# Kernel tuning notes

Measured on AMD Instinct MI355X. Metric: run time of the kernel, lower is better.

Reference implementation:

```python
import jax, jax.numpy as jnp
import numpy as np

MAX_LEN_PROP = 0.75
SCORE_STDDEV = 3.0


def setup_inputs() -> dict:
    key = jax.random.key(0)
    k0, k1, k2, k3, k4, k5 = jax.random.split(key, 6)
    F, B, C = 4096, 32, 512
    x = jax.random.normal(k0, (F, B, C), dtype=jnp.float32)
    lengths = jax.random.randint(k1, (B,), 0, F, dtype=jnp.int32)
    rand_u = jax.random.uniform(k2, (F // 2, B, 1), dtype=jnp.float32)
    W = jax.random.normal(k3, (2, C), dtype=jnp.float32) * 0.02
    b = jax.random.normal(k4, (2,), dtype=jnp.float32) * 0.02
    is_sep = jax.random.normal(k5, (C,), dtype=jnp.float32) * 0.01
    return {"x": x, "lengths": lengths, "rand_u": rand_u, "W": W, "b": b, "is_sep": is_sep}


def reference(x, lengths, rand_u, W, b, is_sep):
    F, B, C = x.shape
    newF = int(1 + F * MAX_LEN_PROP)

    # per-pair loss prediction on even frames: (F/2, B, 2)
    pred = jnp.einsum('fbc,oc->fbo', x[0::2], W) + b

    # normalize scores to target stddev (std over frame axis), negate
    centered = pred - jnp.mean(pred, axis=-1, keepdims=True)
    std = jnp.sqrt(jnp.mean(centered ** 2, axis=0, keepdims=True) + 1e-20)
    scores = centered * (-SCORE_STDDEV / std)
    probs = jax.nn.softmax(scores, axis=-1)

    kept = probs[..., 0:1] > rand_u                       # (F/2, B, 1) bool
    sel = (~kept).astype(jnp.int32)                       # gather index: 0 if kept else 1
    seq_losses = jnp.take_along_axis(pred, sel, axis=2)[..., 0].sum(axis=0)  # (B,)

    lengths_mask = jnp.arange(F)[:, None, None] < lengths[None, :, None]     # (F, B, 1)
    ones = lengths_mask.astype(jnp.int32)
    ones = ones.at[0::2].multiply(kept.astype(jnp.int32))  # drop non-kept even frames

    indexes = jnp.cumsum(ones, axis=0)                     # inclusive cumsum (F, B, 1)
    new_lengths = jnp.minimum(indexes[-1, :, 0], newF)     # (B,)
    indexes = indexes - ones                               # exclusive cumsum = write index

    ones_f = ones.astype(x.dtype)
    pair_mean = ones_f.reshape(F // 2, 2, B, 1).mean(axis=1, keepdims=True)
    scales = jnp.broadcast_to(pair_mean, (F // 2, 2, B, 1)).reshape(F, B, 1)
    scales = jnp.where(indexes >= newF, jnp.zeros((), x.dtype), scales)

    idx = jnp.minimum(indexes, newF - 1)[..., 0]           # (F, B)
    bidx = jnp.arange(B)[None, :]

    # scatter-add compacted, scaled frames into shrunk buffer
    y = jnp.zeros((newF, B, C), x.dtype).at[idx, bidx].add(x * scales)

    kept_dup = jnp.broadcast_to(kept.reshape(F // 2, 1, B, 1), (F // 2, 2, B, 1)).reshape(F, B, 1)
    kept_dup = kept_dup.astype(x.dtype) * lengths_mask.astype(x.dtype)
    is_sep_acc = jnp.zeros((newF, B), x.dtype).at[idx, bidx].add(kept_dup[..., 0])

    y = y + is_sep_acc[..., None] * is_sep
    return y, new_lengths, seq_losses
```

## Files before the change

kernel.cpp:

```cpp
#include <hip/hip_runtime.h>
#include <math.h>

#define FF 4096
#define NPAIR 2048
#define BB 32
#define CC 512
#define NEWF 3073

typedef float f32x4 __attribute__((ext_vector_type(4)));

__global__ __launch_bounds__(256) void pred_kernel(
    const float* __restrict__ x, const float* __restrict__ W,
    const float* __restrict__ bias, double* __restrict__ pred) {
  int wave = threadIdx.x >> 6;
  int lane = threadIdx.x & 63;
  int row  = blockIdx.x * 4 + wave;
  int f2 = row >> 5;
  int b  = row & 31;
  const float* xr = x + ((size_t)(2 * f2) * BB + b) * CC;

  double s0 = 0.0, s1 = 0.0;
#pragma unroll
  for (int k = 0; k < 2; ++k) {
    int c = lane * 4 + k * 256;
    f32x4 xv = *(const f32x4*)(xr + c);
    f32x4 w0 = *(const f32x4*)(W + c);
    f32x4 w1 = *(const f32x4*)(W + CC + c);
    s0 += (double)xv.x * (double)w0.x + (double)xv.y * (double)w0.y +
          (double)xv.z * (double)w0.z + (double)xv.w * (double)w0.w;
    s1 += (double)xv.x * (double)w1.x + (double)xv.y * (double)w1.y +
          (double)xv.z * (double)w1.z + (double)xv.w * (double)w1.w;
  }
#pragma unroll
  for (int off = 32; off; off >>= 1) {
    s0 += __shfl_down(s0, off, 64);
    s1 += __shfl_down(s1, off, 64);
  }
  if (lane == 0) {
    size_t o = ((size_t)b * NPAIR + f2) * 2;
    pred[o + 0] = s0 + (double)bias[0];
    pred[o + 1] = s1 + (double)bias[1];
  }
}

__global__ __launch_bounds__(1024) void scan_kernel(
    const double* __restrict__ pred, const float* __restrict__ rand_u,
    const int* __restrict__ lengths, int* __restrict__ rec,
    int* __restrict__ tail, float* __restrict__ out_tail) {
  int b = blockIdx.x;
  int t = threadIdx.x;
  int lane = t & 63, wid = t >> 6;

  __shared__ double wdbl[16];
  __shared__ int    wint[16];
  __shared__ double s_invs;

  int len = lengths[b];
  const double* pb = pred + (size_t)b * NPAIR * 2;

  int pr0 = 2 * t, pr1 = 2 * t + 1;
  double2 a0 = ((const double2*)pb)[2 * t];
  double2 a1 = ((const double2*)pb)[2 * t + 1];
  float ru0 = rand_u[(size_t)pr0 * BB + b];
  float ru1 = rand_u[(size_t)pr1 * BB + b];
  double d0 = a0.x - a0.y;
  double d1 = a1.x - a1.y;

  double sumsq = 0.25 * (d0 * d0 + d1 * d1);
#pragma unroll
  for (int off = 32; off; off >>= 1) sumsq += __shfl_down(sumsq, off, 64);
  if (lane == 0) wdbl[wid] = sumsq;
  __syncthreads();
  if (t == 0) {
    double s = 0;
#pragma unroll
    for (int i = 0; i < 16; ++i) s += wdbl[i];
    s_invs = -3.0 / sqrt(s / (double)NPAIR + 1e-20);
  }
  __syncthreads();
  double si = s_invs;

  double prob0 = 1.0 / (1.0 + exp(-d0 * si));
  double prob1 = 1.0 / (1.0 + exp(-d1 * si));
  bool kept0 = prob0 > (double)ru0;
  bool kept1 = prob1 > (double)ru1;
  bool oe0 = (2 * pr0 < len) && kept0;
  bool oo0 = (2 * pr0 + 1) < len;
  bool oe1 = (2 * pr1 < len) && kept1;
  bool oo1 = (2 * pr1 + 1) < len;
  int cnt = (int)oe0 + (int)oo0 + (int)oe1 + (int)oo1;

  int sc = cnt;
#pragma unroll
  for (int off = 1; off < 64; off <<= 1) {
    int v = __shfl_up(sc, off, 64);
    if (lane >= off) sc += v;
  }
  if (lane == 63) wint[wid] = sc;
  __syncthreads();
  int wprefix = 0, total = 0;
#pragma unroll
  for (int i = 0; i < 16; ++i) {
    int wv = wint[i];
    if (i < wid) wprefix += wv;
    total += wv;
  }
  int base = wprefix + sc - cnt;

  int* rrow = rec + (size_t)b * NEWF;
  int zstart = total < NEWF ? total : NEWF;
  for (int s = zstart + t; s < NEWF; s += 1024) rrow[s] = 0;
  __syncthreads();

  int excl = base;
  int tailc = 0;
  double seq = (kept0 ? a0.x : a0.y) + (kept1 ? a1.x : a1.y);

#pragma unroll
  for (int i = 0; i < 2; ++i) {
    int pr = 2 * t + i;
    bool kept = i ? kept1 : kept0;
    bool oe = i ? oe1 : oe0;
    bool oo = i ? oo1 : oo0;
    int fe = 2 * pr, fo = fe + 1;
    int excl_e = excl; excl += (int)oe;
    int excl_o = excl; excl += (int)oo;

    if (oe) {
      if (excl_e < NEWF) {
        int half = oo ? 0 : 1;
        rrow[excl_e] = 1 | (half << 2) | (1 << 3) | (fe << 4);
      }
      if (excl_e >= NEWF - 1) tailc++;
    }
    if (oo) {
      if (excl_o < NEWF) {
        int two  = kept ? 0 : 1;
        int half = kept ? 0 : 1;
        rrow[excl_o] = 1 | (two << 1) | (half << 2) | ((kept ? 1 : 0) << 3) | (fo << 4);
      }
      if (kept && excl_o >= NEWF - 1) tailc++;
    }
    if (!oo && oe && excl_o < NEWF) {
      rrow[excl_o] = 1 | (1 << 2) | (fo << 4);
    }
  }

#pragma unroll
  for (int off = 32; off; off >>= 1) {
    seq   += __shfl_down(seq, off, 64);
    tailc += __shfl_down(tailc, off, 64);
  }
  __syncthreads();
  if (lane == 0) { wdbl[wid] = seq; wint[wid] = tailc; }
  __syncthreads();
  if (t == 0) {
    double ss = 0; int tc = 0;
#pragma unroll
    for (int i = 0; i < 16; ++i) { ss += wdbl[i]; tc += wint[i]; }
    tail[b] = tc;
    out_tail[b]      = (float)(total < NEWF ? total : NEWF);
    out_tail[BB + b] = (float)ss;
  }
}

__global__ __launch_bounds__(128) void gather_kernel(
    const float* __restrict__ x, const int* __restrict__ rec,
    const int* __restrict__ tail, const float* __restrict__ is_sep,
    float* __restrict__ y) {
  int s = blockIdx.x;
  int b = blockIdx.y;
  int r = rec[(size_t)b * NEWF + s];
  int c = threadIdx.x * 4;

  int cv = (s == NEWF - 1) ? tail[b] : ((r >> 3) & 1);

  f32x4 acc = (f32x4)(0.f);
  if (r & 1) {
    int f = r >> 4;
    float sc = (r & 4) ? 0.5f : 1.0f;
    f32x4 xv = *(const f32x4*)(x + ((size_t)f * BB + b) * CC + c);
    acc = sc * xv;
    if (r & 2) {
      f32x4 x2 = *(const f32x4*)(x + ((size_t)(f - 1) * BB + b) * CC + c);
      acc += 0.5f * x2;
    }
  }
  if (cv) {
    f32x4 is = *(const f32x4*)(is_sep + c);
    acc += (float)cv * is;
  }
  __builtin_nontemporal_store(acc, (f32x4*)(y + ((size_t)s * BB + b) * CC + c));
}

extern "C" void kernel_launch(void* const* d_in, const int* in_sizes, int n_in,
                              void* d_out, int out_size, void* d_ws, size_t ws_size,
                              hipStream_t stream) {
  (void)in_sizes; (void)n_in; (void)out_size; (void)ws_size;
  const float* x       = (const float*)d_in[0];
  const int*   lengths = (const int*)d_in[1];
  const float* rand_u  = (const float*)d_in[2];
  const float* W       = (const float*)d_in[3];
  const float* bias    = (const float*)d_in[4];
  const float* is_sep  = (const float*)d_in[5];

  float* y = (float*)d_out;
  float* out_tail = y + (size_t)NEWF * BB * CC;

  char* ws = (char*)d_ws;
  double* pred = (double*)ws;
  int* rec  = (int*)(ws + (size_t)BB * NPAIR * 2 * sizeof(double));
  int* tail = rec + (size_t)BB * NEWF;

  pred_kernel<<<(NPAIR * BB) / 4, 256, 0, stream>>>(x, W, bias, pred);
  scan_kernel<<<BB, 1024, 0, stream>>>(pred, rand_u, lengths, rec, tail, out_tail);
  gather_kernel<<<dim3(NEWF, BB), 128, 0, stream>>>(x, rec, tail, is_sep, y);
}
```

Measured before the change: 75.07 us.

## Fuse pred, scan and gather into one persistent cooperative kernel

Merges the three launches into one cooperative kernel that computes predictions grid-stride, syncs the grid, runs the per-batch scan on 32 blocks, syncs again, then gathers output rows in a persistent loop. It is meant to remove launch gaps and inter-kernel idle time. In exchange, most blocks idle during the scan, grid-wide barriers add cost, and the persistent gather loop may keep fewer memory requests in flight. The old three-kernel path remains as a fallback if the cooperative launch fails.

After: 223.4 us. 198% more time.

```diff
diff --git a/kernel.cpp b/kernel.cpp
--- a/kernel.cpp
+++ b/kernel.cpp
@@ -1,13 +1,206 @@
 #include <hip/hip_runtime.h>
+#include <hip/hip_cooperative_groups.h>
 #include <math.h>
+
+namespace cg = cooperative_groups;
 
 #define FF 4096
 #define NPAIR 2048
 #define BB 32
 #define CC 512
 #define NEWF 3073
+#define NROWS (NPAIR * BB)
+#define TPB 256
 
 typedef float f32x4 __attribute__((ext_vector_type(4)));
+
+__device__ inline double dot4d(f32x4 a, f32x4 w) {
+  return (double)a.x * (double)w.x + (double)a.y * (double)w.y +
+         (double)a.z * (double)w.z + (double)a.w * (double)w.w;
+}
+
+__global__ __launch_bounds__(TPB, 2) void fused_kernel(
+    const float* __restrict__ x, const int* __restrict__ lengths,
+    const float* __restrict__ rand_u, const float* __restrict__ W,
+    const float* __restrict__ bias, const float* __restrict__ is_sep,
+    double* __restrict__ pred, int* __restrict__ rec, int* __restrict__ tail,
+    float* __restrict__ y, float* __restrict__ out_tail) {
+  cg::grid_group grid = cg::this_grid();
+  int bid = blockIdx.x;
+  int tid = threadIdx.x;
+  int lane = tid & 63;
+  int wid = tid >> 6;
+
+  {
+    int c0 = lane * 4, c1 = lane * 4 + 256;
+    f32x4 w00 = *(const f32x4*)(W + c0);
+    f32x4 w01 = *(const f32x4*)(W + c1);
+    f32x4 w10 = *(const f32x4*)(W + CC + c0);
+    f32x4 w11 = *(const f32x4*)(W + CC + c1);
+    double bb0 = (double)bias[0], bb1 = (double)bias[1];
+    int nw = gridDim.x * 4;
+    int wgid = bid * 4 + wid;
+    for (int row = wgid; row < NROWS; row += nw) {
+      int f2 = row >> 5, b = row & 31;
+      const float* xr = x + ((size_t)(2 * f2) * BB + b) * CC;
+      f32x4 xv0 = *(const f32x4*)(xr + c0);
+      f32x4 xv1 = *(const f32x4*)(xr + c1);
+      double s0 = dot4d(xv0, w00) + dot4d(xv1, w01);
+      double s1 = dot4d(xv0, w10) + dot4d(xv1, w11);
+#pragma unroll
+      for (int off = 32; off; off >>= 1) {
+        s0 += __shfl_down(s0, off, 64);
+        s1 += __shfl_down(s1, off, 64);
+      }
+      if (lane == 0) {
+        double2 pv; pv.x = s0 + bb0; pv.y = s1 + bb1;
+        ((double2*)pred)[(size_t)b * NPAIR + f2] = pv;
+      }
+    }
+  }
+  grid.sync();
+
+  if (bid < BB) {
+    __shared__ double sh_d[4];
+    __shared__ int    sh_i[4];
+    __shared__ int    sh_s[4];
+    __shared__ double s_invs;
+    int b = bid;
+    int len = lengths[b];
+    const double* pb = pred + (size_t)b * NPAIR * 2;
+
+    double d[8];
+    double sumsq = 0.0;
+#pragma unroll
+    for (int i = 0; i < 8; ++i) {
+      double2 a = ((const double2*)pb)[tid * 8 + i];
+      d[i] = a.x - a.y;
+      sumsq += 0.25 * d[i] * d[i];
+    }
+#pragma unroll
+    for (int off = 32; off; off >>= 1) sumsq += __shfl_down(sumsq, off, 64);
+    if (lane == 0) sh_d[wid] = sumsq;
+    __syncthreads();
+    if (tid == 0)
+      s_invs = -3.0 / sqrt((sh_d[0] + sh_d[1] + sh_d[2] + sh_d[3]) /
+                               (double)NPAIR + 1e-20);
+    __syncthreads();
+    double si = s_invs;
+
+    int keptm = 0, oem = 0, oom = 0, cnt = 0;
+#pragma unroll
+    for (int i = 0; i < 8; ++i) {
+      int pr = tid * 8 + i;
+      double prob = 1.0 / (1.0 + exp(-d[i] * si));
+      bool kept = prob > (double)rand_u[(size_t)pr * BB + b];
+      bool oe = (2 * pr < len) && kept;
+      bool oo = (2 * pr + 1) < len;
+      if (kept) keptm |= 1 << i;
+      if (oe) oem |= 1 << i;
+      if (oo) oom |= 1 << i;
+      cnt += (int)oe + (int)oo;
+    }
+
+    int sc = cnt;
+#pragma unroll
+    for (int off = 1; off < 64; off <<= 1) {
+      int v = __shfl_up(sc, off, 64);
+      if (lane >= off) sc += v;
+    }
+    if (lane == 63) sh_s[wid] = sc;
+    __syncthreads();
+    int wpre = 0, total = 0;
+#pragma unroll
+    for (int i = 0; i < 4; ++i) {
+      if (i < wid) wpre += sh_s[i];
+      total += sh_s[i];
+    }
+    int base = wpre + sc - cnt;
+
+    int* rrow = rec + (size_t)b * NEWF;
+    int zstart = total < NEWF ? total : NEWF;
+    for (int s = zstart + tid; s < NEWF; s += TPB) rrow[s] = 0;
+    __syncthreads();
+
+    int excl = base, tailc = 0;
+    double seq = 0.0;
+#pragma unroll
+    for (int i = 0; i < 8; ++i) {
+      int pr = tid * 8 + i;
+      double2 a = ((const double2*)pb)[pr];
+      bool kept = (keptm >> i) & 1;
+      bool oe = (oem >> i) & 1;
+      bool oo = (oom >> i) & 1;
+      seq += kept ? a.x : a.y;
+      int fe = 2 * pr, fo = fe + 1;
+      int excl_e = excl; excl += (int)oe;
+      int excl_o = excl; excl += (int)oo;
+
+      if (oe) {
+        if (excl_e < NEWF) {
+          int half = oo ? 0 : 1;
+          rrow[excl_e] = 1 | (half << 2) | (1 << 3) | (fe << 4);
+        }
+        if (excl_e >= NEWF - 1) tailc++;
+      }
+      if (oo) {
+        if (excl_o < NEWF) {
+          int two  = kept ? 0 : 1;
+          int half = kept ? 0 : 1;
+          rrow[excl_o] = 1 | (two << 1) | (half << 2) | ((kept ? 1 : 0) << 3) | (fo << 4);
+        }
+        if (kept && excl_o >= NEWF - 1) tailc++;
+      }
+      if (!oo && oe && excl_o < NEWF) {
+        rrow[excl_o] = 1 | (1 << 2) | (fo << 4);
+      }
+    }
+
+#pragma unroll
+    for (int off = 32; off; off >>= 1) {
+      seq   += __shfl_down(seq, off, 64);
+      tailc += __shfl_down(tailc, off, 64);
+    }
+    __syncthreads();
+    if (lane == 0) { sh_d[wid] = seq; sh_i[wid] = tailc; }
+    __syncthreads();
+    if (tid == 0) {
+      tail[b] = sh_i[0] + sh_i[1] + sh_i[2] + sh_i[3];
+      out_tail[b]      = (float)(total < NEWF ? total : NEWF);
+      out_tail[BB + b] = (float)(sh_d[0] + sh_d[1] + sh_d[2] + sh_d[3]);
+    }
+  }
+  grid.sync();
+
+  {
+    int nh = gridDim.x * 2;
+    int hid = bid * 2 + (tid >> 7);
+    int c = (tid & 127) * 4;
+    f32x4 isv = *(const f32x4*)(is_sep + c);
+    int b = 0, s = hid;
+    while (b < BB) {
+      int r = rec[(size_t)b * NEWF + s];
+      int cv = (s == NEWF - 1) ? tail[b] : ((r >> 3) & 1);
+
+      f32x4 acc = (f32x4)(0.f);
+      if (r & 1) {
+        int f = r >> 4;
+        float scv = (r & 4) ? 0.5f : 1.0f;
+        f32x4 xv = *(const f32x4*)(x + ((size_t)f * BB + b) * CC + c);
+        acc = scv * xv;
+        if (r & 2) {
+          f32x4 x2 = *(const f32x4*)(x + ((size_t)(f - 1) * BB + b) * CC + c);
+          acc += 0.5f * x2;
+        }
+      }
+      if (cv) acc += (float)cv * isv;
+      __builtin_nontemporal_store(acc, (f32x4*)(y + ((size_t)s * BB + b) * CC + c));
+
+      s += nh;
+      if (s >= NEWF) { s -= NEWF; b++; }
+    }
+  }
+}
 
 __global__ __launch_bounds__(256) void pred_kernel(
     const float* __restrict__ x, const float* __restrict__ W,
@@ -26,10 +219,8 @@
     f32x4 xv = *(const f32x4*)(xr + c);
     f32x4 w0 = *(const f32x4*)(W + c);
     f32x4 w1 = *(const f32x4*)(W + CC + c);
-    s0 += (double)xv.x * (double)w0.x + (double)xv.y * (double)w0.y +
-          (double)xv.z * (double)w0.z + (double)xv.w * (double)w0.w;
-    s1 += (double)xv.x * (double)w1.x + (double)xv.y * (double)w1.y +
-          (double)xv.z * (double)w1.z + (double)xv.w * (double)w1.w;
+    s0 += dot4d(xv, w0);
+    s1 += dot4d(xv, w1);
   }
 #pragma unroll
   for (int off = 32; off; off >>= 1) {
@@ -178,9 +369,9 @@
   f32x4 acc = (f32x4)(0.f);
   if (r & 1) {
     int f = r >> 4;
-    float sc = (r & 4) ? 0.5f : 1.0f;
+    float scv = (r & 4) ? 0.5f : 1.0f;
     f32x4 xv = *(const f32x4*)(x + ((size_t)f * BB + b) * CC + c);
-    acc = sc * xv;
+    acc = scv * xv;
     if (r & 2) {
       f32x4 x2 = *(const f32x4*)(x + ((size_t)(f - 1) * BB + b) * CC + c);
       acc += 0.5f * x2;
@@ -212,7 +403,31 @@
   int* rec  = (int*)(ws + (size_t)BB * NPAIR * 2 * sizeof(double));
   int* tail = rec + (size_t)BB * NEWF;
 
-  pred_kernel<<<(NPAIR * BB) / 4, 256, 0, stream>>>(x, W, bias, pred);
-  scan_kernel<<<BB, 1024, 0, stream>>>(pred, rand_u, lengths, rec, tail, out_tail);
-  gather_kernel<<<dim3(NEWF, BB), 128, 0, stream>>>(x, rec, tail, is_sep, y);
-}
+  int maxB = 0;
+  hipError_t qe = hipOccupancyMaxActiveBlocksPerMultiprocessor(
+      &maxB, (const void*)fused_kernel, TPB, 0);
+  int grid = 0;
+  if (qe == hipSuccess && maxB > 0) {
+    grid = maxB * 256;
+    if (grid > 512) grid = 512;
+  }
+
+  bool done = false;
+  if (grid >= BB) {
+    void* args[] = {
+      (void*)&x, (void*)&lengths, (void*)&rand_u, (void*)&W, (void*)&bias,
+      (void*)&is_sep, (void*)&pred, (void*)&rec, (void*)&tail, (void*)&y,
+      (void*)&out_tail
+    };
+    hipError_t le = hipLaunchCooperativeKernel((const void*)fused_kernel,
+                                               dim3(grid), dim3(TPB), args, 0,
+                                               stream);
+    done = (le == hipSuccess);
+  }
+
+  if (!done) {
+    pred_kernel<<<(NPAIR * BB) / 4, 256, 0, stream>>>(x, W, bias, pred);
+    scan_kernel<<<BB, 1024, 0, stream>>>(pred, rand_u, lengths, rec, tail, out_tail);
+    gather_kernel<<<dim3(NEWF, BB), 128, 0, stream>>>(x, rec, tail, is_sep, y);
+  }
+}
```
